# Kernel optimization log

Hardware: AMD Instinct MI355X
Metric: run time of the kernel (lower is better)

The kernel has to match this reference:

```python
import jax, jax.numpy as jnp
import numpy as np
from jax import lax

D_MODEL, D_INNER, D_STATE, DT_RANK, K = 96, 192, 16, 6, 4
B_, H_, W_ = 8, 64, 64

def setup_inputs() -> dict:
    key = jax.random.key(0)
    ks = jax.random.split(key, 12)
    return {
        "x": jax.random.normal(ks[0], (B_, H_, W_, D_MODEL), jnp.float32),
        "in_proj_w": jax.random.normal(ks[1], (2 * D_INNER, D_MODEL), jnp.float32) * 0.05,
        "conv_w": jax.random.normal(ks[2], (D_INNER, 1, 3, 3), jnp.float32) * 0.1,
        "conv_b": jax.random.normal(ks[3], (D_INNER,), jnp.float32) * 0.01,
        "x_proj_w": jax.random.normal(ks[4], (K, DT_RANK + 2 * D_STATE, D_INNER), jnp.float32) * 0.05,
        "dt_proj_w": jax.random.normal(ks[5], (K, D_INNER, DT_RANK), jnp.float32) * 0.1,
        "dt_proj_b": jax.random.normal(ks[6], (K, D_INNER), jnp.float32) * 0.1,
        "A_logs": jax.random.uniform(ks[7], (K * D_INNER, D_STATE), jnp.float32, 0.0, 2.0),
        "Ds": jnp.ones((K * D_INNER,), jnp.float32),
        "ln_g": jnp.ones((D_INNER,), jnp.float32),
        "ln_b": jnp.zeros((D_INNER,), jnp.float32),
        "out_proj_w": jax.random.normal(ks[8], (D_MODEL, D_INNER), jnp.float32) * 0.05,
    }

def _selective_scan(xs, delta, A, Bs, Cs, Dk):
    # xs/delta: (B,K,D,L); A: (K,D,N); Bs/Cs: (B,K,N,L); Dk: (K,D)
    u_t = xs.transpose(3, 0, 1, 2)      # (L,B,K,D)
    d_t = delta.transpose(3, 0, 1, 2)   # (L,B,K,D)
    B_t = Bs.transpose(3, 0, 1, 2)      # (L,B,K,N)
    C_t = Cs.transpose(3, 0, 1, 2)      # (L,B,K,N)
    b = xs.shape[0]
    h0 = jnp.zeros((b, K, D_INNER, D_STATE), xs.dtype)
    def step(h, inp):
        ul, dl, Bl, Cl = inp
        dA = jnp.exp(dl[..., None] * A)                 # (B,K,D,N)
        h = dA * h + (dl * ul)[..., None] * Bl[:, :, None, :]
        y = jnp.einsum('bkdn,bkn->bkd', h, Cl)
        return h, y
    _, ys = lax.scan(step, h0, (u_t, d_t, B_t, C_t))
    y = ys.transpose(1, 2, 3, 0)                         # (B,K,D,L)
    return y + xs * Dk[None, :, :, None]

def reference(x, in_proj_w, conv_w, conv_b, x_proj_w, dt_proj_w, dt_proj_b,
              A_logs, Ds, ln_g, ln_b, out_proj_w):
    B, H, W, C = x.shape
    L = H * W
    xz = jnp.einsum('bhwc,ec->bhwe', x, in_proj_w)       # (B,H,W,2*D_inner)
    xc, z = jnp.split(xz, 2, axis=-1)
    xc = xc.transpose(0, 3, 1, 2)                        # (B,D,H,W)
    xc = lax.conv_general_dilated(xc, conv_w, (1, 1), 'SAME',
                                  dimension_numbers=('NCHW', 'OIHW', 'NCHW'),
                                  feature_group_count=D_INNER)
    xa = jax.nn.silu(xc + conv_b[None, :, None, None])
    x_flat = xa.reshape(B, D_INNER, L)
    x_wh = xa.transpose(0, 1, 3, 2).reshape(B, D_INNER, L)
    x_hwwh = jnp.stack([x_flat, x_wh], axis=1)           # (B,2,D,L)
    xs = jnp.concatenate([x_hwwh, jnp.flip(x_hwwh, -1)], axis=1)  # (B,4,D,L)
    x_dbl = jnp.einsum('bkdl,kcd->bkcl', xs, x_proj_w)
    dts = x_dbl[:, :, :DT_RANK]
    Bs = x_dbl[:, :, DT_RANK:DT_RANK + D_STATE]
    Cs = x_dbl[:, :, DT_RANK + D_STATE:]
    dts = jnp.einsum('bkrl,kdr->bkdl', dts, dt_proj_w)
    delta = jax.nn.softplus(dts + dt_proj_b[None, :, :, None])
    A = -jnp.exp(A_logs).reshape(K, D_INNER, D_STATE)
    Dk = Ds.reshape(K, D_INNER)
    out_y = _selective_scan(xs, delta, A, Bs, Cs, Dk)    # (B,4,D,L)
    y1 = out_y[:, 0]
    inv = jnp.flip(out_y[:, 2:4], -1)
    y2 = inv[:, 0]
    y3 = out_y[:, 1].reshape(B, D_INNER, W, H).transpose(0, 1, 3, 2).reshape(B, D_INNER, L)
    y4 = inv[:, 1].reshape(B, D_INNER, W, H).transpose(0, 1, 3, 2).reshape(B, D_INNER, L)
    y = (y1 + y2 + y3 + y4).transpose(0, 2, 1).reshape(B, H, W, D_INNER)
    mu = y.mean(-1, keepdims=True)
    var = ((y - mu) ** 2).mean(-1, keepdims=True)
    y = (y - mu) * lax.rsqrt(var + 1e-5) * ln_g + ln_b
    y = y * jax.nn.silu(z)
    return jnp.einsum('bhwd,cd->bhwc', y, out_proj_w)
```

## Files before the change

### kernel.cpp

```cpp
#include <hip/hip_runtime.h>

#define B_  8
#define L_  4096
#define DI  192
#define LOG2E 1.44269504f
#define LN2F  0.69314718f

#if __has_builtin(__builtin_amdgcn_exp2f)
#define EXP2(x) __builtin_amdgcn_exp2f(x)
#else
#define EXP2(x) __expf((x)*LN2F)
#endif

__global__ __launch_bounds__(256) void k_inproj(
    const float* __restrict__ x, const float* __restrict__ w,
    float* __restrict__ xc, float* __restrict__ z)
{
  __shared__ float As[96*68];
  __shared__ float Ws[96*68];
  const int t  = threadIdx.x;
  const int m0 = blockIdx.x * 64;
  const int n0 = blockIdx.y * 64;
  for (int i = t; i < 64*24; i += 256) {
    const int row = i / 24, q = (i % 24) * 4;
    const float4 v = *(const float4*)&x[(size_t)(m0+row)*96 + q];
    As[(q+0)*68 + row] = v.x; As[(q+1)*68 + row] = v.y;
    As[(q+2)*68 + row] = v.z; As[(q+3)*68 + row] = v.w;
  }
  for (int i = t; i < 64*24; i += 256) {
    const int row = i / 24, q = (i % 24) * 4;
    const float4 v = *(const float4*)&w[(size_t)(n0+row)*96 + q];
    Ws[(q+0)*68 + row] = v.x; Ws[(q+1)*68 + row] = v.y;
    Ws[(q+2)*68 + row] = v.z; Ws[(q+3)*68 + row] = v.w;
  }
  __syncthreads();
  const int tx = t & 15, ty = t >> 4;
  float acc[4][4] = {};
#pragma unroll 4
  for (int kk = 0; kk < 96; ++kk) {
    const float4 a4 = *(const float4*)&As[kk*68 + ty*4];
    const float4 b4 = *(const float4*)&Ws[kk*68 + tx*4];
    const float a[4] = {a4.x, a4.y, a4.z, a4.w};
    const float b[4] = {b4.x, b4.y, b4.z, b4.w};
#pragma unroll
    for (int i = 0; i < 4; ++i)
#pragma unroll
      for (int j = 0; j < 4; ++j) acc[i][j] = fmaf(a[i], b[j], acc[i][j]);
  }
#pragma unroll
  for (int i = 0; i < 4; ++i) {
    const int row = m0 + ty*4 + i;
#pragma unroll
    for (int j = 0; j < 4; ++j) {
      const int col = n0 + tx*4 + j;
      if (col < DI) xc[(size_t)row*DI + col]      = acc[i][j];
      else          z [(size_t)row*DI + col - DI] = acc[i][j];
    }
  }
}

__global__ __launch_bounds__(192) void k_conv(
    const float* __restrict__ xc, const float* __restrict__ cw,
    const float* __restrict__ cb, float* __restrict__ xa)
{
  const int blk = blockIdx.x;
  const int wg = blk & 3, h = (blk >> 2) & 63, b = blk >> 8;
  const int d  = threadIdx.x;
  float wreg[9];
#pragma unroll
  for (int i = 0; i < 9; ++i) wreg[i] = cw[d*9 + i];
  const float bias = cb[d];
  const float* base = xc + ((size_t)(b) << 12)*DI + d;
  const int w0 = wg * 16;
  const bool hm = (h > 0), hp = (h < 63);
  auto LD = [&](int hh, int ww, bool ok) -> float {
    return ok ? base[(size_t)((hh << 6) + ww)*DI] : 0.f;
  };
  float a0 = LD(h-1, w0-1, hm && w0 > 0);
  float a1 = LD(h,   w0-1, w0 > 0);
  float a2 = LD(h+1, w0-1, hp && w0 > 0);
  float b0 = LD(h-1, w0, hm);
  float b1 = LD(h,   w0, true);
  float b2 = LD(h+1, w0, hp);
  float* op = xa + ((size_t)((b << 12) + (h << 6) + w0))*DI + d;
#pragma unroll 4
  for (int w = w0; w < w0 + 16; ++w) {
    const bool wp = (w < 63);
    const float c0 = LD(h-1, w+1, hm && wp);
    const float c1 = LD(h,   w+1, wp);
    const float c2 = LD(h+1, w+1, hp && wp);
    float acc = bias;
    acc = fmaf(a0, wreg[0], acc); acc = fmaf(b0, wreg[1], acc); acc = fmaf(c0, wreg[2], acc);
    acc = fmaf(a1, wreg[3], acc); acc = fmaf(b1, wreg[4], acc); acc = fmaf(c1, wreg[5], acc);
    acc = fmaf(a2, wreg[6], acc); acc = fmaf(b2, wreg[7], acc); acc = fmaf(c2, wreg[8], acc);
    const float sig = 1.f / (1.f + __expf(-acc));
    *op = acc * sig;
    op += DI;
    a0 = b0; a1 = b1; a2 = b2;
    b0 = c0; b1 = c1; b2 = c2;
  }
}

#define WSL(c,q) ((c)*36 + ((((q) ^ (((c)>>2)&7)) & 7) << 2))
__global__ __launch_bounds__(256) void k_xproj(
    const float* __restrict__ xa, const float* __restrict__ xw,
    float* __restrict__ proj)
{
  __shared__ float V[64*196];
  __shared__ float W[152*36];
  const int t  = threadIdx.x;
  const int s0 = blockIdx.x * 64;
  for (int i = t; i < 64*48; i += 256) {
    const int row = i / 48;
    const int q   = (i % 48) * 4;
    *(float4*)&V[row*196 + q] = *(const float4*)&xa[(size_t)(s0+row)*192 + q];
  }
  const int tx = t & 15;
  const int ty = t >> 4;
  const int c0 = tx * 10;
  float acc[4][10] = {};
#pragma unroll 1
  for (int p = 0; p < 6; ++p) {
    __syncthreads();
    for (int i = t; i < 152*8; i += 256) {
      const int c = i >> 3, q = i & 7;
      *(float4*)&W[WSL(c,q)] = *(const float4*)&xw[(size_t)c*192 + p*32 + q*4];
    }
    __syncthreads();
#pragma unroll
    for (int rs = 0; rs < 8; ++rs) {
      const int r0 = p*32 + rs*4;
      float av[4][4];
#pragma unroll
      for (int m = 0; m < 4; ++m) {
        const float4 a4 = *(const float4*)&V[(ty*4+m)*196 + r0];
        av[m][0]=a4.x; av[m][1]=a4.y; av[m][2]=a4.z; av[m][3]=a4.w;
      }
      float wr[10][4];
#pragma unroll
      for (int j = 0; j < 10; ++j) {
        const int cg = (c0 + j < 152) ? c0 + j : 151;
        const float4 w4 = *(const float4*)&W[WSL(cg,rs)];
        wr[j][0]=w4.x; wr[j][1]=w4.y; wr[j][2]=w4.z; wr[j][3]=w4.w;
      }
#pragma unroll
      for (int i = 0; i < 4; ++i)
#pragma unroll
        for (int m = 0; m < 4; ++m)
#pragma unroll
          for (int j = 0; j < 10; ++j)
            acc[m][j] = fmaf(av[m][i], wr[j][i], acc[m][j]);
    }
  }
  __syncthreads();
  float* Csm = V;
#pragma unroll
  for (int m = 0; m < 4; ++m)
#pragma unroll
    for (int j = 0; j < 10; ++j)
      if (c0 + j < 152) Csm[(ty*4+m)*162 + c0 + j] = acc[m][j];
  __syncthreads();
  const int b = s0 >> 12;
  const int sbase = s0 & 4095;
#pragma unroll 1
  for (int k = 0; k < 4; ++k) {
    float* op = proj + ((size_t)((b<<2)+k)*L_ + sbase)*40;
#pragma unroll
    for (int it = 0; it < 10; ++it) {
      const int f = it*256 + t;
      const int s = f / 40, c = f - s*40;
      op[f] = (c < 38) ? Csm[s*162 + k*38 + c] : 0.f;
    }
  }
}

template<int NC>
__global__ __launch_bounds__(192) void k_scan1(
    const float* __restrict__ xa, const float* __restrict__ proj,
    const float* __restrict__ alog, const float* __restrict__ dtw,
    const float* __restrict__ dtb,
    float* __restrict__ P, float* __restrict__ Hl)
{
  constexpr int CL = L_ / NC;
  const int blk = blockIdx.x;
  const int c = blk % NC, b = blk / (NC*4);
  const int k = ((blk / NC) + b) & 3;
  const int d = threadIdx.x;
  const int kd = k*DI + d;
  const int rev = (k >> 1) & 1, sw = k & 1;
  float A2[16], dw[6];
#pragma unroll
  for (int n = 0; n < 16; ++n) A2[n] = -__expf(alog[kd*16 + n]) * LOG2E;
#pragma unroll
  for (int r = 0; r < 6; ++r) dw[r] = dtw[kd*6 + r];
  const float db = dtb[kd];
  float h[16];
#pragma unroll
  for (int n = 0; n < 16; ++n) h[n] = 0.f;
  float Sd = 0.f;
  const int l0 = c * CL;
  const int l2_0 = rev ? 4095 - l0 : l0;
  const int sbase = sw ? (((l2_0 & 63) << 6) | (l2_0 >> 6)) : l2_0;
  const int stp = sw ? (rev ? -64 : 64) : (rev ? -1 : 1);
  const float* up = xa + ((size_t)(b << 12) + sbase)*DI + d;
  const char* pr8 = (const char*)(proj + ((((size_t)((b<<2)+k)) << 12) + sbase)*40);
  const ptrdiff_t ustep = (ptrdiff_t)stp * DI;
  const ptrdiff_t pstepB = (ptrdiff_t)stp * 160;
  const size_t obase = ((size_t)((b*4 + k)*NC + c)) * 16 * DI + d;
#pragma unroll 2
  for (int t = 0; t < CL; ++t) {
    const float u = *up;
    const float4 q0 = *(const float4*)(pr8 +  0);
    const float4 q1 = *(const float4*)(pr8 + 16);
    const float4 q2 = *(const float4*)(pr8 + 32);
    const float4 q3 = *(const float4*)(pr8 + 48);
    const float4 q4 = *(const float4*)(pr8 + 64);
    const float4 q5 = *(const float4*)(pr8 + 80);
    float xdt = db;
    xdt = fmaf(dw[0], q0.x, xdt); xdt = fmaf(dw[1], q0.y, xdt);
    xdt = fmaf(dw[2], q0.z, xdt); xdt = fmaf(dw[3], q0.w, xdt);
    xdt = fmaf(dw[4], q1.x, xdt); xdt = fmaf(dw[5], q1.y, xdt);
    const float delta = (xdt > 20.f) ? xdt
                       : LN2F * __log2f(1.f + EXP2(xdt * LOG2E));
    Sd += delta;
    const float du = delta * u;
    const float Bv[16] = {q1.z,q1.w,q2.x,q2.y,q2.z,q2.w,q3.x,q3.y,
                          q3.z,q3.w,q4.x,q4.y,q4.z,q4.w,q5.x,q5.y};
#pragma unroll
    for (int n = 0; n < 16; ++n) {
      const float dA = EXP2(delta * A2[n]);
      h[n] = fmaf(dA, h[n], du * Bv[n]);
    }
    up += ustep; pr8 += pstepB;
  }
#pragma unroll
  for (int n = 0; n < 16; ++n) {
    P[obase + n*DI]  = EXP2(A2[n] * Sd);
    Hl[obase + n*DI] = h[n];
  }
}

template<int NC, bool ZERO>
__global__ __launch_bounds__(256) void k_scan2(
    const float* P, const float* __restrict__ Hl, float* hin,
    float* __restrict__ ycomb)
{
  const int tid = blockIdx.x * 256 + threadIdx.x;
  if (ZERO)
    for (size_t i = tid; i < (size_t)B_*L_*DI; i += 98304) ycomb[i] = 0.f;
  const int d  = tid % DI;
  const int n  = (tid / DI) & 15;
  const int bk = tid / (DI*16);
  float h = 0.f;
  for (int cc = 0; cc < NC; ++cc) {
    const size_t idx = ((size_t)(bk*NC + cc)*16 + n)*DI + d;
    const float pv = P[idx];
    const float hl = Hl[idx];
    hin[idx] = h;
    h = fmaf(pv, h, hl);
  }
}

template<int NC>
__global__ __launch_bounds__(192) void k_scan3f(
    const float* __restrict__ xa, const float* __restrict__ proj,
    const float* __restrict__ alog, const float* __restrict__ dtw,
    const float* __restrict__ dtb, const float* __restrict__ Dv,
    const float* __restrict__ hin,
    float* __restrict__ y0, float* __restrict__ y1,
    float* __restrict__ y2, float* __restrict__ y3)
{
  constexpr int CL = L_ / NC;
  const int blk = blockIdx.x;
  const int c = blk % NC, b = blk / (NC*4);
  const int k = ((blk / NC) + b) & 3;
  const int d = threadIdx.x;
  const int kd = k*DI + d;
  const int rev = (k >> 1) & 1, sw = k & 1;
  float A2[16], dw[6];
#pragma unroll
  for (int n = 0; n < 16; ++n) A2[n] = -__expf(alog[kd*16 + n]) * LOG2E;
#pragma unroll
  for (int r = 0; r < 6; ++r) dw[r] = dtw[kd*6 + r];
  const float db = dtb[kd];
  const float Dd = Dv[kd];
  float h[16];
  const size_t base = ((size_t)((b*4 + k)*NC + c)) * 16 * DI + d;
#pragma unroll
  for (int n = 0; n < 16; ++n) h[n] = hin[base + n*DI];
  const int l0 = c * CL;
  const int l2_0 = rev ? 4095 - l0 : l0;
  const int sbase = sw ? (((l2_0 & 63) << 6) | (l2_0 >> 6)) : l2_0;
  const int stp = sw ? (rev ? -64 : 64) : (rev ? -1 : 1);
  const float* up = xa + ((size_t)(b << 12) + sbase)*DI + d;
  const char* pr8 = (const char*)(proj + ((((size_t)((b<<2)+k)) << 12) + sbase)*40);
  const ptrdiff_t ustep = (ptrdiff_t)stp * DI;
  const ptrdiff_t pstepB = (ptrdiff_t)stp * 160;
  float* yb = (k == 0) ? y0 : (k == 1) ? y1 : (k == 2) ? y2 : y3;
  float* yp = yb + ((size_t)(b << 12) + l2_0)*DI + d;
  const ptrdiff_t ystep = (ptrdiff_t)(rev ? -1 : 1) * DI;
#pragma unroll 2
  for (int t = 0; t < CL; ++t) {
    const float u = *up;
    const float4 q0 = *(const float4*)(pr8 +   0);
    const float4 q1 = *(const float4*)(pr8 +  16);
    const float4 q2 = *(const float4*)(pr8 +  32);
    const float4 q3 = *(const float4*)(pr8 +  48);
    const float4 q4 = *(const float4*)(pr8 +  64);
    const float4 q5 = *(const float4*)(pr8 +  80);
    const float4 q6 = *(const float4*)(pr8 +  96);
    const float4 q7 = *(const float4*)(pr8 + 112);
    const float4 q8 = *(const float4*)(pr8 + 128);
    const float4 q9 = *(const float4*)(pr8 + 144);
    float xdt = db;
    xdt = fmaf(dw[0], q0.x, xdt); xdt = fmaf(dw[1], q0.y, xdt);
    xdt = fmaf(dw[2], q0.z, xdt); xdt = fmaf(dw[3], q0.w, xdt);
    xdt = fmaf(dw[4], q1.x, xdt); xdt = fmaf(dw[5], q1.y, xdt);
    const float delta = (xdt > 20.f) ? xdt
                       : LN2F * __log2f(1.f + EXP2(xdt * LOG2E));
    const float du = delta * u;
    const float Bv[16] = {q1.z,q1.w,q2.x,q2.y,q2.z,q2.w,q3.x,q3.y,
                          q3.z,q3.w,q4.x,q4.y,q4.z,q4.w,q5.x,q5.y};
    const float Cv[16] = {q5.z,q5.w,q6.x,q6.y,q6.z,q6.w,q7.x,q7.y,
                          q7.z,q7.w,q8.x,q8.y,q8.z,q8.w,q9.x,q9.y};
    float y = 0.f;
#pragma unroll
    for (int n = 0; n < 16; ++n) {
      const float dA = EXP2(delta * A2[n]);
      h[n] = fmaf(dA, h[n], du * Bv[n]);
      y = fmaf(h[n], Cv[n], y);
    }
    y = fmaf(u, Dd, y);
    *yp = y;
    yp += ystep; up += ustep; pr8 += pstepB;
  }
}

template<int NC>
__global__ __launch_bounds__(192) void k_scan3a(
    const float* __restrict__ xa, const float* __restrict__ proj,
    const float* __restrict__ alog, const float* __restrict__ dtw,
    const float* __restrict__ dtb, const float* __restrict__ Dv,
    const float* __restrict__ hin, float* __restrict__ ycomb)
{
  constexpr int CL = L_ / NC;
  const int blk = blockIdx.x;
  const int c = blk % NC, b = blk / (NC*4);
  const int k = ((blk / NC) + b) & 3;
  const int d = threadIdx.x;
  const int kd = k*DI + d;
  const int rev = (k >> 1) & 1, sw = k & 1;
  float A2[16], dw[6];
#pragma unroll
  for (int n = 0; n < 16; ++n) A2[n] = -__expf(alog[kd*16 + n]) * LOG2E;
#pragma unroll
  for (int r = 0; r < 6; ++r) dw[r] = dtw[kd*6 + r];
  const float db = dtb[kd];
  const float Dd = Dv[kd];
  float h[16];
  const size_t base = ((size_t)((b*4 + k)*NC + c)) * 16 * DI + d;
#pragma unroll
  for (int n = 0; n < 16; ++n) h[n] = hin[base + n*DI];
  const int l0 = c * CL;
  const float* xab = xa + (size_t)(b << 12)*DI + d;
  const float* pb  = proj + (((size_t)((b<<2)+k)) << 12)*40;
#pragma unroll 2
  for (int t = 0; t < CL; ++t) {
    const int l = l0 + t;
    const int l2 = rev ? 4095 - l : l;
    const int s  = sw ? (((l2 & 63) << 6) | (l2 >> 6)) : l2;
    const float u = xab[(size_t)s*DI];
    const float* pp = pb + (size_t)s*40;
    float xdt = db;
#pragma unroll
    for (int r = 0; r < 6; ++r) xdt = fmaf(dw[r], pp[r], xdt);
    const float delta = (xdt > 20.f) ? xdt : __logf(1.f + __expf(xdt));
    const float du = delta * u;
    float y = 0.f;
#pragma unroll
    for (int n = 0; n < 16; ++n) {
      const float dA = EXP2(delta * A2[n]);
      h[n] = fmaf(dA, h[n], du * pp[6+n]);
      y = fmaf(h[n], pp[22+n], y);
    }
    y = fmaf(u, Dd, y);
    atomicAdd(&ycomb[(size_t)((b<<12) + s)*DI + d], y);
  }
}

template<int MODE>
__global__ __launch_bounds__(256) void k_final(
    const float* __restrict__ y0, const float* __restrict__ y1,
    const float* __restrict__ y2, const float* __restrict__ y3,
    const float* __restrict__ zb,
    const float* __restrict__ lng, const float* __restrict__ lnb,
    const float* __restrict__ ow, float* __restrict__ out)
{
  __shared__ float yt[192*68];
  __shared__ float W2[96*36];
  const int t = threadIdx.x;
  const int lane = t & 63, wv = t >> 6;
  const int g0 = blockIdx.x * 64;
  for (int si = 0; si < 16; ++si) {
    const int sl = wv*16 + si;
    const int g  = g0 + sl;
    const int s  = g & 4095;
    const size_t r13 = (size_t)(g & ~4095) | (((s & 63) << 6) | (s >> 6));
    float v[3]; float sum = 0.f, sq = 0.f;
#pragma unroll
    for (int j = 0; j < 3; ++j) {
      const int ch = lane*3 + j;
      float vv = y0[(size_t)g*DI + ch];
      if (MODE == 0)
        vv += y2[(size_t)g*DI + ch] + y1[r13*DI + ch] + y3[r13*DI + ch];
      v[j] = vv;
      sum += vv; sq = fmaf(vv, vv, sq);
    }
#pragma unroll
    for (int o = 1; o < 64; o <<= 1) { sum += __shfl_xor(sum, o); sq += __shfl_xor(sq, o); }
    const float mu = sum * (1.f/192.f);
    const float rs = rsqrtf(sq*(1.f/192.f) - mu*mu + 1e-5f);
#pragma unroll
    for (int j = 0; j < 3; ++j) {
      const int ch = lane*3 + j;
      const float zv = zb[(size_t)g*DI + ch];
      const float sz = zv / (1.f + __expf(-zv));
      yt[ch*68 + sl] = ((v[j]-mu)*rs*lng[ch] + lnb[ch]) * sz;
    }
  }
  __syncthreads();
  const int tx = t & 15, ty = t >> 4;
  const int c0 = tx*6;
  float acc[4][6] = {};
#pragma unroll 1
  for (int p = 0; p < 6; ++p) {
    if (p) __syncthreads();
    for (int i = t; i < 96*8; i += 256) {
      const int c = i >> 3, q = i & 7;
      *(float4*)&W2[WSL(c,q)] = *(const float4*)&ow[(size_t)c*192 + p*32 + q*4];
    }
    __syncthreads();
#pragma unroll
    for (int rs = 0; rs < 8; ++rs) {
      const int k4 = p*32 + rs*4;
      float4 bw[6];
#pragma unroll
      for (int j = 0; j < 6; ++j) bw[j] = *(const float4*)&W2[WSL(c0+j, rs)];
#pragma unroll
      for (int i4 = 0; i4 < 4; ++i4) {
        const float4 a4 = *(const float4*)&yt[(k4+i4)*68 + ty*4];
        const float av[4] = {a4.x, a4.y, a4.z, a4.w};
        const float bv[6] = {
          i4==0?bw[0].x:i4==1?bw[0].y:i4==2?bw[0].z:bw[0].w,
          i4==0?bw[1].x:i4==1?bw[1].y:i4==2?bw[1].z:bw[1].w,
          i4==0?bw[2].x:i4==1?bw[2].y:i4==2?bw[2].z:bw[2].w,
          i4==0?bw[3].x:i4==1?bw[3].y:i4==2?bw[3].z:bw[3].w,
          i4==0?bw[4].x:i4==1?bw[4].y:i4==2?bw[4].z:bw[4].w,
          i4==0?bw[5].x:i4==1?bw[5].y:i4==2?bw[5].z:bw[5].w };
#pragma unroll
        for (int i = 0; i < 4; ++i)
#pragma unroll
          for (int j = 0; j < 6; ++j) acc[i][j] = fmaf(av[i], bv[j], acc[i][j]);
      }
    }
  }
#pragma unroll
  for (int i = 0; i < 4; ++i) {
    const size_t row = (size_t)(g0 + ty*4 + i)*96 + c0;
#pragma unroll
    for (int j = 0; j < 6; ++j) out[row + j] = acc[i][j];
  }
}

extern "C" void kernel_launch(void* const* d_in, const int* in_sizes, int n_in,
                              void* d_out, int out_size, void* d_ws, size_t ws_size,
                              hipStream_t stream)
{
  (void)in_sizes; (void)n_in; (void)out_size;
  const float* x    = (const float*)d_in[0];
  const float* ipw  = (const float*)d_in[1];
  const float* cw   = (const float*)d_in[2];
  const float* cb   = (const float*)d_in[3];
  const float* xpw  = (const float*)d_in[4];
  const float* dpw  = (const float*)d_in[5];
  const float* dpb  = (const float*)d_in[6];
  const float* alog = (const float*)d_in[7];
  const float* Dv   = (const float*)d_in[8];
  const float* lng  = (const float*)d_in[9];
  const float* lnb  = (const float*)d_in[10];
  const float* opw  = (const float*)d_in[11];
  float* out = (float*)d_out;

  float* ws    = (float*)d_ws;
  float* xc    = ws;
  float* zbuf  = ws + 6291456;
  float* xa    = ws + 12582912;
  float* proj  = ws + 18874368;
  float* after = ws + 24117248;
  const size_t YSZ = 6291456;

  k_inproj<<<dim3(512, 6), 256, 0, stream>>>(x, ipw, xc, zbuf);
  k_conv  <<<2048, 192, 0, stream>>>(xc, cw, cb, xa);
  k_xproj <<<512, 256, 0, stream>>>(xa, xpw, proj);

  const size_t needF64  = (24117248ull + 2ull*98304*64  + 2*YSZ) * 4;
  const size_t needB    = 30408704ull * 4;

  if (ws_size >= needF64) {
    constexpr int NC = 64;
    float* Pb  = after;
    float* Hlb = after + (size_t)98304*NC;
    float* y1  = Hlb;
    float* y2  = after + 2ull*98304*NC;
    float* y3  = y2 + YSZ;
    k_scan1<NC><<<8*4*NC, 192, 0, stream>>>(xa, proj, alog, dpw, dpb, Pb, Hlb);
    k_scan2<NC,false><<<384, 256, 0, stream>>>(Pb, Hlb, Pb, nullptr);
    k_scan3f<NC><<<8*4*NC, 192, 0, stream>>>(xa, proj, alog, dpw, dpb, Dv, Pb, xc, y1, y2, y3);
    k_final<0><<<512, 256, 0, stream>>>(xc, y1, y2, y3, zbuf, lng, lnb, opw, out);
  } else if (ws_size >= needB) {
    constexpr int NC = 32;
    float* Pb  = after;
    float* Hlb = after + (size_t)98304*NC;
    k_scan1<NC><<<8*4*NC, 192, 0, stream>>>(xa, proj, alog, dpw, dpb, Pb, Hlb);
    k_scan2<NC,true><<<384, 256, 0, stream>>>(Pb, Hlb, Pb, xc);
    k_scan3a<NC><<<8*4*NC, 192, 0, stream>>>(xa, proj, alog, dpw, dpb, Dv, Pb, xc);
    k_final<1><<<512, 256, 0, stream>>>(xc, nullptr, nullptr, nullptr, zbuf, lng, lnb, opw, out);
  } else {
    constexpr int NC = 16;
    float* Pb  = after;
    float* Hlb = after + (size_t)98304*NC;
    k_scan1<NC><<<8*4*NC, 192, 0, stream>>>(xa, proj, alog, dpw, dpb, Pb, Hlb);
    k_scan2<NC,true><<<384, 256, 0, stream>>>(Pb, Hlb, Pb, xc);
    k_scan3a<NC><<<8*4*NC, 192, 0, stream>>>(xa, proj, alog, dpw, dpb, Dv, Pb, xc);
    k_final<1><<<512, 256, 0, stream>>>(xc, nullptr, nullptr, nullptr, zbuf, lng, lnb, opw, out);
  }
}
```

Measured before the change: 337.8 us.

## Store transposed conv output and scan-order projections for contiguous scan access

The conv kernel now also writes a transposed (W-major) copy of its activations, and x_proj scatters the projections for the odd (column-order) directions into scan order. The scan kernels can then stride by one row in every direction instead of jumping 64 rows apart, and they write y1/y3 back in spatial order so the final kernel reads all four outputs with the same index. The chunk count is also raised to 128 when the workspace allows it, giving more blocks. The cost is an extra full activation write, scattered writes in x_proj, and more workspace.

New measurement: 355.6 us. +5.3%, slower.

```diff
diff --git a/kernel.cpp b/kernel.cpp
--- a/kernel.cpp
+++ b/kernel.cpp
@@ -59,9 +59,11 @@
   }
 }
 
+template<bool TR>
 __global__ __launch_bounds__(192) void k_conv(
     const float* __restrict__ xc, const float* __restrict__ cw,
-    const float* __restrict__ cb, float* __restrict__ xa)
+    const float* __restrict__ cb, float* __restrict__ xa,
+    float* __restrict__ xa_t)
 {
   const int blk = blockIdx.x;
   const int wg = blk & 3, h = (blk >> 2) & 63, b = blk >> 8;
@@ -82,7 +84,8 @@
   float b0 = LD(h-1, w0, hm);
   float b1 = LD(h,   w0, true);
   float b2 = LD(h+1, w0, hp);
-  float* op = xa + ((size_t)((b << 12) + (h << 6) + w0))*DI + d;
+  float* op  = xa + ((size_t)((b << 12) + (h << 6) + w0))*DI + d;
+  float* opT = TR ? xa_t + ((size_t)((b << 12) + (w0 << 6) + h))*DI + d : nullptr;
 #pragma unroll 4
   for (int w = w0; w < w0 + 16; ++w) {
     const bool wp = (w < 63);
@@ -94,7 +97,9 @@
     acc = fmaf(a1, wreg[3], acc); acc = fmaf(b1, wreg[4], acc); acc = fmaf(c1, wreg[5], acc);
     acc = fmaf(a2, wreg[6], acc); acc = fmaf(b2, wreg[7], acc); acc = fmaf(c2, wreg[8], acc);
     const float sig = 1.f / (1.f + __expf(-acc));
-    *op = acc * sig;
+    const float val = acc * sig;
+    *op = val;
+    if (TR) { *opT = val; opT += 64*DI; }
     op += DI;
     a0 = b0; a1 = b1; a2 = b2;
     b0 = c0; b1 = c1; b2 = c2;
@@ -102,6 +107,7 @@
 }
 
 #define WSL(c,q) ((c)*36 + ((((q) ^ (((c)>>2)&7)) & 7) << 2))
+template<bool TRANS>
 __global__ __launch_bounds__(256) void k_xproj(
     const float* __restrict__ xa, const float* __restrict__ xw,
     float* __restrict__ proj)
@@ -162,15 +168,183 @@
   __syncthreads();
   const int b = s0 >> 12;
   const int sbase = s0 & 4095;
+  const int hh = sbase >> 6;
 #pragma unroll 1
   for (int k = 0; k < 4; ++k) {
-    float* op = proj + ((size_t)((b<<2)+k)*L_ + sbase)*40;
+    const bool scat = TRANS && (k & 1);
+    float* opb = proj + (size_t)((b<<2)+k)*L_*40;
 #pragma unroll
     for (int it = 0; it < 10; ++it) {
       const int f = it*256 + t;
       const int s = f / 40, c = f - s*40;
-      op[f] = (c < 38) ? Csm[s*162 + k*38 + c] : 0.f;
-    }
+      const int row = scat ? ((s << 6) | hh) : (sbase + s);
+      opb[(size_t)row*40 + c] = (c < 38) ? Csm[s*162 + k*38 + c] : 0.f;
+    }
+  }
+}
+
+template<int NC>
+__global__ __launch_bounds__(192) void k_scan1t(
+    const float* __restrict__ xa, const float* __restrict__ xa_t,
+    const float* __restrict__ proj,
+    const float* __restrict__ alog, const float* __restrict__ dtw,
+    const float* __restrict__ dtb,
+    float* __restrict__ P, float* __restrict__ Hl)
+{
+  constexpr int CL = L_ / NC;
+  const int blk = blockIdx.x;
+  const int c = blk % NC, b = blk / (NC*4);
+  const int k = ((blk / NC) + b) & 3;
+  const int d = threadIdx.x;
+  const int kd = k*DI + d;
+  const int rev = (k >> 1) & 1;
+  float A2[16], dw[6];
+#pragma unroll
+  for (int n = 0; n < 16; ++n) A2[n] = -__expf(alog[kd*16 + n]) * LOG2E;
+#pragma unroll
+  for (int r = 0; r < 6; ++r) dw[r] = dtw[kd*6 + r];
+  const float db = dtb[kd];
+  float h[16];
+#pragma unroll
+  for (int n = 0; n < 16; ++n) h[n] = 0.f;
+  float Sd = 0.f;
+  const int l0 = c * CL;
+  const int idx0 = rev ? 4095 - l0 : l0;
+  const int stride = rev ? -1 : 1;
+  const float* usrc = (k & 1) ? xa_t : xa;
+  const float* up = usrc + ((size_t)(b << 12) + idx0)*DI + d;
+  const char* pr8 = (const char*)(proj + ((((size_t)((b<<2)+k)) << 12) + idx0)*40);
+  const ptrdiff_t ustep = (ptrdiff_t)stride * DI;
+  const ptrdiff_t pstepB = (ptrdiff_t)stride * 160;
+  const size_t obase = ((size_t)((b*4 + k)*NC + c)) * 16 * DI + d;
+#pragma unroll 2
+  for (int t = 0; t < CL; ++t) {
+    const float u = *up;
+    const float4 q0 = *(const float4*)(pr8 +  0);
+    const float4 q1 = *(const float4*)(pr8 + 16);
+    const float4 q2 = *(const float4*)(pr8 + 32);
+    const float4 q3 = *(const float4*)(pr8 + 48);
+    const float4 q4 = *(const float4*)(pr8 + 64);
+    const float4 q5 = *(const float4*)(pr8 + 80);
+    float xdt = db;
+    xdt = fmaf(dw[0], q0.x, xdt); xdt = fmaf(dw[1], q0.y, xdt);
+    xdt = fmaf(dw[2], q0.z, xdt); xdt = fmaf(dw[3], q0.w, xdt);
+    xdt = fmaf(dw[4], q1.x, xdt); xdt = fmaf(dw[5], q1.y, xdt);
+    const float delta = (xdt > 20.f) ? xdt
+                       : LN2F * __log2f(1.f + EXP2(xdt * LOG2E));
+    Sd += delta;
+    const float du = delta * u;
+    const float Bv[16] = {q1.z,q1.w,q2.x,q2.y,q2.z,q2.w,q3.x,q3.y,
+                          q3.z,q3.w,q4.x,q4.y,q4.z,q4.w,q5.x,q5.y};
+#pragma unroll
+    for (int n = 0; n < 16; ++n) {
+      const float dA = EXP2(delta * A2[n]);
+      h[n] = fmaf(dA, h[n], du * Bv[n]);
+    }
+    up += ustep; pr8 += pstepB;
+  }
+#pragma unroll
+  for (int n = 0; n < 16; ++n) {
+    P[obase + n*DI]  = EXP2(A2[n] * Sd);
+    Hl[obase + n*DI] = h[n];
+  }
+}
+
+template<int NC, bool ZERO>
+__global__ __launch_bounds__(256) void k_scan2(
+    const float* P, const float* __restrict__ Hl, float* hin,
+    float* __restrict__ ycomb)
+{
+  const int tid = blockIdx.x * 256 + threadIdx.x;
+  if (ZERO)
+    for (size_t i = tid; i < (size_t)B_*L_*DI; i += 98304) ycomb[i] = 0.f;
+  const int d  = tid % DI;
+  const int n  = (tid / DI) & 15;
+  const int bk = tid / (DI*16);
+  float h = 0.f;
+  for (int cc = 0; cc < NC; ++cc) {
+    const size_t idx = ((size_t)(bk*NC + cc)*16 + n)*DI + d;
+    const float pv = P[idx];
+    const float hl = Hl[idx];
+    hin[idx] = h;
+    h = fmaf(pv, h, hl);
+  }
+}
+
+template<int NC>
+__global__ __launch_bounds__(192) void k_scan3t(
+    const float* __restrict__ xa, const float* __restrict__ xa_t,
+    const float* __restrict__ proj,
+    const float* __restrict__ alog, const float* __restrict__ dtw,
+    const float* __restrict__ dtb, const float* __restrict__ Dv,
+    const float* __restrict__ hin,
+    float* __restrict__ y0, float* __restrict__ y1,
+    float* __restrict__ y2, float* __restrict__ y3)
+{
+  constexpr int CL = L_ / NC;
+  const int blk = blockIdx.x;
+  const int c = blk % NC, b = blk / (NC*4);
+  const int k = ((blk / NC) + b) & 3;
+  const int d = threadIdx.x;
+  const int kd = k*DI + d;
+  const int rev = (k >> 1) & 1;
+  float A2[16], dw[6];
+#pragma unroll
+  for (int n = 0; n < 16; ++n) A2[n] = -__expf(alog[kd*16 + n]) * LOG2E;
+#pragma unroll
+  for (int r = 0; r < 6; ++r) dw[r] = dtw[kd*6 + r];
+  const float db = dtb[kd];
+  const float Dd = Dv[kd];
+  float h[16];
+  const size_t base = ((size_t)((b*4 + k)*NC + c)) * 16 * DI + d;
+#pragma unroll
+  for (int n = 0; n < 16; ++n) h[n] = hin[base + n*DI];
+  const int l0 = c * CL;
+  const int idx0 = rev ? 4095 - l0 : l0;
+  const int stride = rev ? -1 : 1;
+  const float* usrc = (k & 1) ? xa_t : xa;
+  const float* up = usrc + ((size_t)(b << 12) + idx0)*DI + d;
+  const char* pr8 = (const char*)(proj + ((((size_t)((b<<2)+k)) << 12) + idx0)*40);
+  const ptrdiff_t ustep = (ptrdiff_t)stride * DI;
+  const ptrdiff_t pstepB = (ptrdiff_t)stride * 160;
+  float* yb = (k == 0) ? y0 : (k == 1) ? y1 : (k == 2) ? y2 : y3;
+  const int site0 = (k & 1) ? (((idx0 & 63) << 6) | (idx0 >> 6)) : idx0;
+  float* yp = yb + ((size_t)(b << 12) + site0)*DI + d;
+  const ptrdiff_t ystep = (ptrdiff_t)stride * ((k & 1) ? 64 : 1) * DI;
+#pragma unroll 2
+  for (int t = 0; t < CL; ++t) {
+    const float u = *up;
+    const float4 q0 = *(const float4*)(pr8 +   0);
+    const float4 q1 = *(const float4*)(pr8 +  16);
+    const float4 q2 = *(const float4*)(pr8 +  32);
+    const float4 q3 = *(const float4*)(pr8 +  48);
+    const float4 q4 = *(const float4*)(pr8 +  64);
+    const float4 q5 = *(const float4*)(pr8 +  80);
+    const float4 q6 = *(const float4*)(pr8 +  96);
+    const float4 q7 = *(const float4*)(pr8 + 112);
+    const float4 q8 = *(const float4*)(pr8 + 128);
+    const float4 q9 = *(const float4*)(pr8 + 144);
+    float xdt = db;
+    xdt = fmaf(dw[0], q0.x, xdt); xdt = fmaf(dw[1], q0.y, xdt);
+    xdt = fmaf(dw[2], q0.z, xdt); xdt = fmaf(dw[3], q0.w, xdt);
+    xdt = fmaf(dw[4], q1.x, xdt); xdt = fmaf(dw[5], q1.y, xdt);
+    const float delta = (xdt > 20.f) ? xdt
+                       : LN2F * __log2f(1.f + EXP2(xdt * LOG2E));
+    const float du = delta * u;
+    const float Bv[16] = {q1.z,q1.w,q2.x,q2.y,q2.z,q2.w,q3.x,q3.y,
+                          q3.z,q3.w,q4.x,q4.y,q4.z,q4.w,q5.x,q5.y};
+    const float Cv[16] = {q5.z,q5.w,q6.x,q6.y,q6.z,q6.w,q7.x,q7.y,
+                          q7.z,q7.w,q8.x,q8.y,q8.z,q8.w,q9.x,q9.y};
+    float y = 0.f;
+#pragma unroll
+    for (int n = 0; n < 16; ++n) {
+      const float dA = EXP2(delta * A2[n]);
+      h[n] = fmaf(dA, h[n], du * Bv[n]);
+      y = fmaf(h[n], Cv[n], y);
+    }
+    y = fmaf(u, Dd, y);
+    *yp = y;
+    yp += ystep; up += ustep; pr8 += pstepB;
   }
 }
 
@@ -240,102 +414,6 @@
   }
 }
 
-template<int NC, bool ZERO>
-__global__ __launch_bounds__(256) void k_scan2(
-    const float* P, const float* __restrict__ Hl, float* hin,
-    float* __restrict__ ycomb)
-{
-  const int tid = blockIdx.x * 256 + threadIdx.x;
-  if (ZERO)
-    for (size_t i = tid; i < (size_t)B_*L_*DI; i += 98304) ycomb[i] = 0.f;
-  const int d  = tid % DI;
-  const int n  = (tid / DI) & 15;
-  const int bk = tid / (DI*16);
-  float h = 0.f;
-  for (int cc = 0; cc < NC; ++cc) {
-    const size_t idx = ((size_t)(bk*NC + cc)*16 + n)*DI + d;
-    const float pv = P[idx];
-    const float hl = Hl[idx];
-    hin[idx] = h;
-    h = fmaf(pv, h, hl);
-  }
-}
-
-template<int NC>
-__global__ __launch_bounds__(192) void k_scan3f(
-    const float* __restrict__ xa, const float* __restrict__ proj,
-    const float* __restrict__ alog, const float* __restrict__ dtw,
-    const float* __restrict__ dtb, const float* __restrict__ Dv,
-    const float* __restrict__ hin,
-    float* __restrict__ y0, float* __restrict__ y1,
-    float* __restrict__ y2, float* __restrict__ y3)
-{
-  constexpr int CL = L_ / NC;
-  const int blk = blockIdx.x;
-  const int c = blk % NC, b = blk / (NC*4);
-  const int k = ((blk / NC) + b) & 3;
-  const int d = threadIdx.x;
-  const int kd = k*DI + d;
-  const int rev = (k >> 1) & 1, sw = k & 1;
-  float A2[16], dw[6];
-#pragma unroll
-  for (int n = 0; n < 16; ++n) A2[n] = -__expf(alog[kd*16 + n]) * LOG2E;
-#pragma unroll
-  for (int r = 0; r < 6; ++r) dw[r] = dtw[kd*6 + r];
-  const float db = dtb[kd];
-  const float Dd = Dv[kd];
-  float h[16];
-  const size_t base = ((size_t)((b*4 + k)*NC + c)) * 16 * DI + d;
-#pragma unroll
-  for (int n = 0; n < 16; ++n) h[n] = hin[base + n*DI];
-  const int l0 = c * CL;
-  const int l2_0 = rev ? 4095 - l0 : l0;
-  const int sbase = sw ? (((l2_0 & 63) << 6) | (l2_0 >> 6)) : l2_0;
-  const int stp = sw ? (rev ? -64 : 64) : (rev ? -1 : 1);
-  const float* up = xa + ((size_t)(b << 12) + sbase)*DI + d;
-  const char* pr8 = (const char*)(proj + ((((size_t)((b<<2)+k)) << 12) + sbase)*40);
-  const ptrdiff_t ustep = (ptrdiff_t)stp * DI;
-  const ptrdiff_t pstepB = (ptrdiff_t)stp * 160;
-  float* yb = (k == 0) ? y0 : (k == 1) ? y1 : (k == 2) ? y2 : y3;
-  float* yp = yb + ((size_t)(b << 12) + l2_0)*DI + d;
-  const ptrdiff_t ystep = (ptrdiff_t)(rev ? -1 : 1) * DI;
-#pragma unroll 2
-  for (int t = 0; t < CL; ++t) {
-    const float u = *up;
-    const float4 q0 = *(const float4*)(pr8 +   0);
-    const float4 q1 = *(const float4*)(pr8 +  16);
-    const float4 q2 = *(const float4*)(pr8 +  32);
-    const float4 q3 = *(const float4*)(pr8 +  48);
-    const float4 q4 = *(const float4*)(pr8 +  64);
-    const float4 q5 = *(const float4*)(pr8 +  80);
-    const float4 q6 = *(const float4*)(pr8 +  96);
-    const float4 q7 = *(const float4*)(pr8 + 112);
-    const float4 q8 = *(const float4*)(pr8 + 128);
-    const float4 q9 = *(const float4*)(pr8 + 144);
-    float xdt = db;
-    xdt = fmaf(dw[0], q0.x, xdt); xdt = fmaf(dw[1], q0.y, xdt);
-    xdt = fmaf(dw[2], q0.z, xdt); xdt = fmaf(dw[3], q0.w, xdt);
-    xdt = fmaf(dw[4], q1.x, xdt); xdt = fmaf(dw[5], q1.y, xdt);
-    const float delta = (xdt > 20.f) ? xdt
-                       : LN2F * __log2f(1.f + EXP2(xdt * LOG2E));
-    const float du = delta * u;
-    const float Bv[16] = {q1.z,q1.w,q2.x,q2.y,q2.z,q2.w,q3.x,q3.y,
-                          q3.z,q3.w,q4.x,q4.y,q4.z,q4.w,q5.x,q5.y};
-    const float Cv[16] = {q5.z,q5.w,q6.x,q6.y,q6.z,q6.w,q7.x,q7.y,
-                          q7.z,q7.w,q8.x,q8.y,q8.z,q8.w,q9.x,q9.y};
-    float y = 0.f;
-#pragma unroll
-    for (int n = 0; n < 16; ++n) {
-      const float dA = EXP2(delta * A2[n]);
-      h[n] = fmaf(dA, h[n], du * Bv[n]);
-      y = fmaf(h[n], Cv[n], y);
-    }
-    y = fmaf(u, Dd, y);
-    *yp = y;
-    yp += ystep; up += ustep; pr8 += pstepB;
-  }
-}
-
 template<int NC>
 __global__ __launch_bounds__(192) void k_scan3a(
     const float* __restrict__ xa, const float* __restrict__ proj,
@@ -404,15 +482,13 @@
   for (int si = 0; si < 16; ++si) {
     const int sl = wv*16 + si;
     const int g  = g0 + sl;
-    const int s  = g & 4095;
-    const size_t r13 = (size_t)(g & ~4095) | (((s & 63) << 6) | (s >> 6));
     float v[3]; float sum = 0.f, sq = 0.f;
 #pragma unroll
     for (int j = 0; j < 3; ++j) {
       const int ch = lane*3 + j;
       float vv = y0[(size_t)g*DI + ch];
       if (MODE == 0)
-        vv += y2[(size_t)g*DI + ch] + y1[r13*DI + ch] + y3[r13*DI + ch];
+        vv += y1[(size_t)g*DI + ch] + y2[(size_t)g*DI + ch] + y3[(size_t)g*DI + ch];
       v[j] = vv;
       sum += vv; sq = fmaf(vv, vv, sq);
     }
@@ -500,35 +576,56 @@
   const size_t YSZ = 6291456;
 
   k_inproj<<<dim3(512, 6), 256, 0, stream>>>(x, ipw, xc, zbuf);
-  k_conv  <<<2048, 192, 0, stream>>>(xc, cw, cb, xa);
-  k_xproj <<<512, 256, 0, stream>>>(xa, xpw, proj);
-
-  const size_t needF64  = (24117248ull + 2ull*98304*64  + 2*YSZ) * 4;
-  const size_t needB    = 30408704ull * 4;
-
-  if (ws_size >= needF64) {
+
+  const size_t needA = (24117248ull + 2ull*98304*128 + 2*YSZ) * 4;
+  const size_t needBt = (24117248ull + 2ull*98304*64 + 3*YSZ) * 4;
+  const size_t needC = (24117248ull + 2ull*98304*64 + 2*YSZ) * 4;
+  const size_t needD = 30408704ull * 4;
+
+  if (ws_size >= needA) {
+    constexpr int NC = 128;
+    float* Pb  = after;
+    float* Hlb = after + (size_t)98304*NC;
+    float* y1  = Hlb;
+    float* y2  = Hlb + YSZ;
+    float* y3  = after + 2ull*98304*NC;
+    float* xaT = y3 + YSZ;
+    k_conv<true><<<2048, 192, 0, stream>>>(xc, cw, cb, xa, xaT);
+    k_xproj<true><<<512, 256, 0, stream>>>(xa, xpw, proj);
+    k_scan1t<NC><<<8*4*NC, 192, 0, stream>>>(xa, xaT, proj, alog, dpw, dpb, Pb, Hlb);
+    k_scan2<NC,false><<<384, 256, 0, stream>>>(Pb, Hlb, Pb, nullptr);
+    k_scan3t<NC><<<8*4*NC, 192, 0, stream>>>(xa, xaT, proj, alog, dpw, dpb, Dv, Pb, xc, y1, y2, y3);
+    k_final<0><<<512, 256, 0, stream>>>(xc, y1, y2, y3, zbuf, lng, lnb, opw, out);
+  } else if (ws_size >= needBt) {
     constexpr int NC = 64;
     float* Pb  = after;
     float* Hlb = after + (size_t)98304*NC;
     float* y1  = Hlb;
     float* y2  = after + 2ull*98304*NC;
     float* y3  = y2 + YSZ;
-    k_scan1<NC><<<8*4*NC, 192, 0, stream>>>(xa, proj, alog, dpw, dpb, Pb, Hlb);
+    float* xaT = y3 + YSZ;
+    k_conv<true><<<2048, 192, 0, stream>>>(xc, cw, cb, xa, xaT);
+    k_xproj<true><<<512, 256, 0, stream>>>(xa, xpw, proj);
+    k_scan1t<NC><<<8*4*NC, 192, 0, stream>>>(xa, xaT, proj, alog, dpw, dpb, Pb, Hlb);
     k_scan2<NC,false><<<384, 256, 0, stream>>>(Pb, Hlb, Pb, nullptr);
-    k_scan3f<NC><<<8*4*NC, 192, 0, stream>>>(xa, proj, alog, dpw, dpb, Dv, Pb, xc, y1, y2, y3);
+    k_scan3t<NC><<<8*4*NC, 192, 0, stream>>>(xa, xaT, proj, alog, dpw, dpb, Dv, Pb, xc, y1, y2, y3);
     k_final<0><<<512, 256, 0, stream>>>(xc, y1, y2, y3, zbuf, lng, lnb, opw, out);
-  } else if (ws_size >= needB) {
-    constexpr int NC = 32;
+  } else if (ws_size >= needC) {
+    constexpr int NC = 64;
     float* Pb  = after;
     float* Hlb = after + (size_t)98304*NC;
+    k_conv<false><<<2048, 192, 0, stream>>>(xc, cw, cb, xa, nullptr);
+    k_xproj<false><<<512, 256, 0, stream>>>(xa, xpw, proj);
     k_scan1<NC><<<8*4*NC, 192, 0, stream>>>(xa, proj, alog, dpw, dpb, Pb, Hlb);
     k_scan2<NC,true><<<384, 256, 0, stream>>>(Pb, Hlb, Pb, xc);
     k_scan3a<NC><<<8*4*NC, 192, 0, stream>>>(xa, proj, alog, dpw, dpb, Dv, Pb, xc);
     k_final<1><<<512, 256, 0, stream>>>(xc, nullptr, nullptr, nullptr, zbuf, lng, lnb, opw, out);
   } else {
-    constexpr int NC = 16;
+    constexpr int NC = 32;
     float* Pb  = after;
     float* Hlb = after + (size_t)98304*NC;
+    k_conv<false><<<2048, 192, 0, stream>>>(xc, cw, cb, xa, nullptr);
+    k_xproj<false><<<512, 256, 0, stream>>>(xa, xpw, proj);
     k_scan1<NC><<<8*4*NC, 192, 0, stream>>>(xa, proj, alog, dpw, dpb, Pb, Hlb);
     k_scan2<NC,true><<<384, 256, 0, stream>>>(Pb, Hlb, Pb, xc);
     k_scan3a<NC><<<8*4*NC, 192, 0, stream>>>(xa, proj, alog, dpw, dpb, Dv, Pb, xc);
```
